# Optimization experiments

Measured on AMD Instinct MI355X. Metric: run time of the kernel, lower is better.

## Reference

```python
import jax, jax.numpy as jnp
import numpy as np

DIM = 192
HEADS = 6
G = 16          # window size (ds_flag=0 dense attention)
B = 1
H_SZ = 256
W_SZ = 256
POS_DIM = 12    # (dim//4)//4
HIDDEN = 768    # 4*dim


def _ln(x, g, b, eps=1e-5):
    m = jnp.mean(x, -1, keepdims=True)
    v = jnp.var(x, -1, keepdims=True)
    return (x - m) / jnp.sqrt(v + eps) * g + b


def setup_inputs() -> dict:
    key = jax.random.key(0)
    ks = jax.random.split(key, 8)
    s = 0.05
    return {
        "x": jax.random.normal(ks[0], (B, H_SZ * W_SZ, DIM), jnp.float32),
        "gamma1": jnp.ones((DIM,), jnp.float32),
        "beta1": jnp.zeros((DIM,), jnp.float32),
        "qkv_w": jax.random.normal(ks[1], (DIM, 3 * DIM), jnp.float32) * s,
        "qkv_b": jnp.zeros((3 * DIM,), jnp.float32),
        "proj_w": jax.random.normal(ks[2], (DIM, DIM), jnp.float32) * s,
        "proj_b": jnp.zeros((DIM,), jnp.float32),
        "pos_proj_w": jax.random.normal(ks[3], (2, POS_DIM), jnp.float32) * s,
        "pos_proj_b": jnp.zeros((POS_DIM,), jnp.float32),
        "ln1_g": jnp.ones((POS_DIM,), jnp.float32),
        "ln1_b": jnp.zeros((POS_DIM,), jnp.float32),
        "pos1_w": jax.random.normal(ks[4], (POS_DIM, POS_DIM), jnp.float32) * s,
        "pos1_b": jnp.zeros((POS_DIM,), jnp.float32),
        "ln2_g": jnp.ones((POS_DIM,), jnp.float32),
        "ln2_b": jnp.zeros((POS_DIM,), jnp.float32),
        "pos2_w": jax.random.normal(ks[5], (POS_DIM, POS_DIM), jnp.float32) * s,
        "pos2_b": jnp.zeros((POS_DIM,), jnp.float32),
        "ln3_g": jnp.ones((POS_DIM,), jnp.float32),
        "ln3_b": jnp.zeros((POS_DIM,), jnp.float32),
        "pos3_w": jax.random.normal(ks[6], (POS_DIM, HEADS), jnp.float32) * s,
        "pos3_b": jnp.zeros((HEADS,), jnp.float32),
        "gamma2": jnp.ones((DIM,), jnp.float32),
        "beta2": jnp.zeros((DIM,), jnp.float32),
        "fc1_w": jax.random.normal(ks[7], (DIM, HIDDEN), jnp.float32) * s,
        "fc1_b": jnp.zeros((HIDDEN,), jnp.float32),
        "fc2_w": jax.random.normal(jax.random.fold_in(key, 9), (HIDDEN, DIM), jnp.float32) * s,
        "fc2_b": jnp.zeros((DIM,), jnp.float32),
        "H": H_SZ,
        "W": W_SZ,
    }


def reference(x, gamma1, beta1, qkv_w, qkv_b, proj_w, proj_b,
              pos_proj_w, pos_proj_b, ln1_g, ln1_b, pos1_w, pos1_b,
              ln2_g, ln2_b, pos2_w, pos2_b, ln3_g, ln3_b, pos3_w, pos3_b,
              gamma2, beta2, fc1_w, fc1_b, fc2_w, fc2_b, H, W):
    Bx, L, C = x.shape
    h = HEADS
    d = C // h
    N = G * G
    shortcut = x
    xn = _ln(x, gamma1, beta1)
    # window partition (H, W divisible by G -> no padding, attn_mask=None)
    xw = xn.reshape(Bx, H // G, G, W // G, G, C).transpose(0, 1, 3, 2, 4, 5)
    xw = xw.reshape(-1, N, C)                       # [B_, N, C]
    B_ = xw.shape[0]
    qkv = (xw @ qkv_w + qkv_b).reshape(B_, N, 3, h, d)
    q = qkv[:, :, 0].transpose(0, 2, 1, 3) * (d ** -0.5)   # [B_, h, N, d]
    k = qkv[:, :, 1].transpose(0, 2, 1, 3)
    v = qkv[:, :, 2].transpose(0, 2, 1, 3)
    attn = jnp.einsum('bhnd,bhmd->bhnm', q, k)      # [B_, h, N, N]
    # dynamic relative position bias (DynamicPosBias MLP + gather)
    r = jnp.arange(1 - G, G)
    biases = jnp.stack(jnp.meshgrid(r, r, indexing='ij')).reshape(2, -1).T.astype(x.dtype)  # [(2G-1)^2, 2]
    p = biases @ pos_proj_w + pos_proj_b
    p = jax.nn.relu(_ln(p, ln1_g, ln1_b)) @ pos1_w + pos1_b
    p = jax.nn.relu(_ln(p, ln2_g, ln2_b)) @ pos2_w + pos2_b
    p = jax.nn.relu(_ln(p, ln3_g, ln3_b)) @ pos3_w + pos3_b  # [(2G-1)^2, heads]
    c = jnp.stack(jnp.meshgrid(jnp.arange(G), jnp.arange(G), indexing='ij')).reshape(2, -1)
    rel = c[:, :, None] - c[:, None, :]             # [2, N, N]
    idx = (rel[0] + G - 1) * (2 * G - 1) + (rel[1] + G - 1)  # [N, N]
    attn = attn + p[idx].transpose(2, 0, 1)[None]   # add [1, h, N, N] bias
    attn = jax.nn.softmax(attn, axis=-1)
    out = jnp.einsum('bhnm,bhmd->bhnd', attn, v).transpose(0, 2, 1, 3).reshape(B_, N, C)
    out = out @ proj_w + proj_b
    # window reverse
    out = out.reshape(Bx, H // G, W // G, G, G, C).transpose(0, 1, 3, 2, 4, 5).reshape(Bx, L, C)
    x = shortcut + out
    y = _ln(x, gamma2, beta2)
    y = jax.nn.gelu(y @ fc1_w + fc1_b, approximate=False) @ fc2_w + fc2_b
    return x + y
```

## Files before the change

### kernel.cpp

```cpp
#include <hip/hip_runtime.h>
#include <hip/hip_bf16.h>

#define DIM 192
#define HEADS 6
#define QKV_N 576
#define HIDDEN 768
#define M_ROWS 65536

typedef unsigned short ushortT;
typedef __attribute__((ext_vector_type(8))) short short8v;
typedef __attribute__((ext_vector_type(4))) float f32x4;
typedef __attribute__((ext_vector_type(4))) unsigned int u32x4;

#define QSCALE_L2E 0.2550348649f
#define LOG2E 1.4426950408889634f

__device__ __forceinline__ float bf2f(ushortT u) {
    union { unsigned int i; float f; } c; c.i = ((unsigned int)u) << 16; return c.f;
}
__device__ __forceinline__ ushortT f2bf(float f) {
    union { float f; unsigned int i; } c; c.f = f;
    unsigned int i = c.i;
    return (ushortT)((i + 0x7fffu + ((i >> 16) & 1u)) >> 16);
}

#define GLOBAL_LOAD_LDS16(gp, lp) \
    __builtin_amdgcn_global_load_lds((const __attribute__((address_space(1))) void*)(gp), \
                                     (__attribute__((address_space(3))) void*)(lp), 16, 0, 0)

__device__ __forceinline__ void ln_relu_mm12(const float* in, const float* g, const float* b,
                                             const float* w, const float* bb, float* out, int nout) {
    float m = 0.f;
#pragma unroll
    for (int j = 0; j < 12; ++j) m += in[j];
    m *= (1.0f / 12.0f);
    float v = 0.f;
#pragma unroll
    for (int j = 0; j < 12; ++j) { float d = in[j] - m; v += d * d; }
    v *= (1.0f / 12.0f);
    float r = rsqrtf(v + 1e-5f);
    float t[12];
#pragma unroll
    for (int j = 0; j < 12; ++j) t[j] = fmaxf((in[j] - m) * r * g[j] + b[j], 0.0f);
    for (int j2 = 0; j2 < nout; ++j2) {
        float s = bb[j2];
#pragma unroll
        for (int j = 0; j < 12; ++j) s = fmaf(t[j], w[j * nout + j2], s);
        out[j2] = s;
    }
}

__global__ __launch_bounds__(256) void prep_kernel(
        const float* __restrict__ qkv_w, const float* __restrict__ proj_w,
        const float* __restrict__ fc1_w, const float* __restrict__ fc2_w,
        ushortT* __restrict__ qkv_wt, ushortT* __restrict__ proj_wt,
        ushortT* __restrict__ fc1_wt, ushortT* __restrict__ fc2_wt,
        const float* __restrict__ pw, const float* __restrict__ pb,
        const float* __restrict__ g1, const float* __restrict__ b1,
        const float* __restrict__ w1, const float* __restrict__ bb1,
        const float* __restrict__ g2, const float* __restrict__ b2,
        const float* __restrict__ w2, const float* __restrict__ bb2,
        const float* __restrict__ g3, const float* __restrict__ b3,
        const float* __restrict__ w3, const float* __restrict__ bb3,
        float* __restrict__ BTf) {
    __shared__ float tile[32][33];
    int blk = blockIdx.x;
    int t = threadIdx.x;
    if (blk < 432) {
        const float* W; ushortT* Wt; int K, N, bx, by;
        if (blk < 108)      { W = qkv_w;  Wt = qkv_wt;  K = 192; N = 576; bx = blk % 18;        by = blk / 18; }
        else if (blk < 144) { int r = blk - 108; W = proj_w; Wt = proj_wt; K = 192; N = 192; bx = r % 6;  by = r / 6; }
        else if (blk < 288) { int r = blk - 144; W = fc1_w;  Wt = fc1_wt;  K = 192; N = 768; bx = r % 24; by = r / 24; }
        else                { int r = blk - 288; W = fc2_w;  Wt = fc2_wt;  K = 768; N = 192; bx = r % 6;  by = r / 6; }
        int tx = t & 31, ty = t >> 5;
        int bX = bx * 32, bY = by * 32;
#pragma unroll
        for (int i = 0; i < 32; i += 8)
            tile[ty + i][tx] = W[(size_t)(bY + ty + i) * N + bX + tx];
        __syncthreads();
#pragma unroll
        for (int i = 0; i < 32; i += 8)
            Wt[(size_t)(bX + ty + i) * K + bY + tx] = f2bf(tile[tx][ty + i]);
    } else {
        int blk2 = blk - 432;
        int h = blk2 >> 8, q = blk2 & 255, kv = t;
        float di = (float)((q >> 4) - (kv >> 4));
        float dj = (float)((q & 15) - (kv & 15));
        float a[12], hh[12];
#pragma unroll
        for (int j = 0; j < 12; ++j) a[j] = di * pw[j] + dj * pw[12 + j] + pb[j];
        ln_relu_mm12(a, g1, b1, w1, bb1, hh, 12);
        ln_relu_mm12(hh, g2, b2, w2, bb2, a, 12);
        float m = 0.f;
#pragma unroll
        for (int j = 0; j < 12; ++j) m += a[j];
        m *= (1.0f / 12.0f);
        float v = 0.f;
#pragma unroll
        for (int j = 0; j < 12; ++j) { float d = a[j] - m; v += d * d; }
        v *= (1.0f / 12.0f);
        float r = rsqrtf(v + 1e-5f);
        float s = bb3[h];
#pragma unroll
        for (int j = 0; j < 12; ++j)
            s = fmaf(fmaxf((a[j] - m) * r * g3[j] + b3[j], 0.0f), w3[j * 6 + h], s);
        int wid = q >> 6, mf = (q >> 4) & 3, l4 = (q >> 2) & 3, rr = q & 3;
        int kc = kv >> 5, cc = kv & 31;
        int cf = (cc >> 4) & 1, l15 = cc & 15;
        int lane = l4 * 16 + l15;
        size_t off = ((size_t)((h * 8 + kc) * 32 + wid * 8 + mf * 2 + cf)) * 256 + lane * 4 + rr;
        BTf[off] = s * LOG2E;
    }
}

__global__ __launch_bounds__(256) void ln_kernel(const float* __restrict__ x,
                                                 const float* __restrict__ g,
                                                 const float* __restrict__ b,
                                                 ushortT* __restrict__ out) {
    int lane = threadIdx.x & 63;
    size_t row = (size_t)blockIdx.x * 4 + (threadIdx.x >> 6);
    const float* xr = x + row * DIM;
    float v0 = xr[lane], v1 = xr[lane + 64], v2 = xr[lane + 128];
    float s = v0 + v1 + v2;
    float ss = v0 * v0 + v1 * v1 + v2 * v2;
#pragma unroll
    for (int off = 32; off > 0; off >>= 1) {
        s += __shfl_xor(s, off);
        ss += __shfl_xor(ss, off);
    }
    float mean = s * (1.0f / DIM);
    float rstd = rsqrtf(ss * (1.0f / DIM) - mean * mean + 1e-5f);
    ushortT* o = out + row * DIM;
    o[lane]       = f2bf((v0 - mean) * rstd * g[lane]       + b[lane]);
    o[lane + 64]  = f2bf((v1 - mean) * rstd * g[lane + 64]  + b[lane + 64]);
    o[lane + 128] = f2bf((v2 - mean) * rstd * g[lane + 128] + b[lane + 128]);
}

template <int MODE, int NY>
__global__ __launch_bounds__(256) void mfma_gemm(const ushortT* __restrict__ A,
                                                 const ushortT* __restrict__ Wt,
                                                 const float* __restrict__ bias,
                                                 const float* __restrict__ resid,
                                                 void* __restrict__ outp,
                                                 int N, int K) {
    __shared__ ushortT As[128 * 64];
    __shared__ ushortT Bs[64 * 64];
    int tid = threadIdx.x;
    int lane = tid & 63, wid = tid >> 6;
    int l15 = lane & 15, l4 = lane >> 4;
    int wr = wid >> 1, wc = wid & 1;
    int p = blockIdx.x;
    int cpx = gridDim.x >> 3;
    int logical = (p & 7) * cpx + (p >> 3);
    int bx = logical / NY;
    int by = logical - bx * NY;
    int bm = bx * 128, bn = by * 64;

    f32x4 acc[4][2];
#pragma unroll
    for (int mf = 0; mf < 4; ++mf)
#pragma unroll
        for (int nf = 0; nf < 2; ++nf)
#pragma unroll
            for (int r = 0; r < 4; ++r) acc[mf][nf][r] = 0.f;

    int srow = tid >> 3;
    int schunk = (tid & 7) ^ (srow & 7);
    const ushortT* agp = A + (size_t)(bm + srow) * K + schunk * 8;
    const ushortT* bgp = Wt + (size_t)(bn + srow) * K + schunk * 8;

    for (int k0 = 0; k0 < K; k0 += 64) {
#pragma unroll
        for (int i = 0; i < 4; ++i)
            GLOBAL_LOAD_LDS16(agp + (size_t)i * 32 * K + k0, As + i * 2048 + wid * 512);
#pragma unroll
        for (int i = 0; i < 2; ++i)
            GLOBAL_LOAD_LDS16(bgp + (size_t)i * 32 * K + k0, Bs + i * 2048 + wid * 512);
        __syncthreads();
#pragma unroll
        for (int ks = 0; ks < 2; ++ks) {
            short8v af[4], bf[2];
#pragma unroll
            for (int mf = 0; mf < 4; ++mf) {
                int row = wr * 64 + mf * 16 + l15;
                af[mf] = *(const short8v*)&As[row * 64 + (((ks * 4 + l4) ^ (l15 & 7)) << 3)];
            }
#pragma unroll
            for (int nf = 0; nf < 2; ++nf) {
                int row = wc * 32 + nf * 16 + l15;
                bf[nf] = *(const short8v*)&Bs[row * 64 + (((ks * 4 + l4) ^ (l15 & 7)) << 3)];
            }
#pragma unroll
            for (int mf = 0; mf < 4; ++mf)
#pragma unroll
                for (int nf = 0; nf < 2; ++nf)
                    acc[mf][nf] = __builtin_amdgcn_mfma_f32_16x16x32_bf16(af[mf], bf[nf], acc[mf][nf], 0, 0, 0);
        }
        __syncthreads();
    }
#pragma unroll
    for (int mf = 0; mf < 4; ++mf) {
        size_t row = (size_t)bm + wr * 64 + mf * 16 + l4 * 4;
#pragma unroll
        for (int nf = 0; nf < 2; ++nf) {
            int col = bn + wc * 32 + nf * 16 + l15;
            float bv = bias[col];
#pragma unroll
            for (int r = 0; r < 4; ++r) {
                size_t off = (row + r) * (size_t)N + col;
                float v = acc[mf][nf][r] + bv;
                if (MODE == 0) {
                    if (col < 192) v *= QSCALE_L2E;
                    ((ushortT*)outp)[off] = f2bf(v);
                } else if (MODE == 1) {
                    float x3 = v * v * v;
                    float z = fmaf(x3, -0.1029537917f, v * -2.302205077f);
                    float e = exp2f(z);
                    v = v * __builtin_amdgcn_rcpf(1.0f + e);
                    ((ushortT*)outp)[off] = f2bf(v);
                } else if (MODE == 2) {
                    ((float*)outp)[off] = resid[off] + v;
                } else {
                    ((float*)outp)[off] += v;
                }
            }
        }
    }
}

__global__ __launch_bounds__(256) void attn_mfma_kernel(const ushortT* __restrict__ qkv,
                                                        const float* __restrict__ BTf,
                                                        ushortT* __restrict__ O) {
    __shared__ ushortT Vt[32][264];
    __shared__ unsigned int Ps[4][64][20];
    int wh = blockIdx.x;
    int w = wh / 6, h = wh - w * 6;
    int wi = w >> 4, wj = w & 15;
    int tid = threadIdx.x, lane = tid & 63, wid = tid >> 6;
    int l15 = lane & 15, l4 = lane >> 4;

    {
        int t = tid;
        int pcol = (t & ~31) | (((t & 15) << 1) | ((t >> 4) & 1));
        size_t gr = (size_t)((wi * 16 + (t >> 4)) * 256 + wj * 16 + (t & 15));
        const ushortT* vp = qkv + gr * 576 + 384 + h * 32;
#pragma unroll
        for (int d0 = 0; d0 < 32; d0 += 8) {
            short8v u = *(const short8v*)(vp + d0);
#pragma unroll
            for (int j = 0; j < 8; ++j) Vt[d0 + j][pcol] = (ushortT)u[j];
        }
    }
    short8v qf[4];
    int qbase = wid * 64;
#pragma unroll
    for (int mf = 0; mf < 4; ++mf) {
        int q = qbase + mf * 16 + l15;
        size_t gr = (size_t)((wi * 16 + (q >> 4)) * 256 + wj * 16 + (q & 15));
        qf[mf] = *(const short8v*)(qkv + gr * 576 + h * 32 + l4 * 8);
    }
    __syncthreads();

    float l_run[4][4];
    f32x4 accO[4][2];
#pragma unroll
    for (int mf = 0; mf < 4; ++mf)
#pragma unroll
        for (int r = 0; r < 4; ++r) {
            l_run[mf][r] = 0.f;
            accO[mf][0][r] = 0.f;
            accO[mf][1][r] = 0.f;
        }
    const float* btb = BTf + ((size_t)(h * 8) * 32 + wid * 8) * 256 + lane * 4;

    auto load_kf = [&](int kc, short8v* kf) {
#pragma unroll
        for (int cf = 0; cf < 2; ++cf) {
            int kv = kc * 32 + cf * 16 + l15;
            size_t gr = (size_t)((wi * 16 + (kv >> 4)) * 256 + wj * 16 + (kv & 15));
            kf[cf] = *(const short8v*)(qkv + gr * 576 + 192 + h * 32 + l4 * 8);
        }
    };

    short8v kfA[2], kfB[2];
    load_kf(0, kfA);

    for (int kc = 0; kc < 8; ++kc) {
        if (kc < 7) load_kf(kc + 1, kfB);
        f32x4 s[4][2];
#pragma unroll
        for (int mf = 0; mf < 4; ++mf)
#pragma unroll
            for (int cf = 0; cf < 2; ++cf)
                s[mf][cf] = *(const f32x4*)(btb + (size_t)(kc * 32 + mf * 2 + cf) * 256);
        __builtin_amdgcn_s_setprio(1);
#pragma unroll
        for (int mf = 0; mf < 4; ++mf)
#pragma unroll
            for (int cf = 0; cf < 2; ++cf)
                s[mf][cf] = __builtin_amdgcn_mfma_f32_16x16x32_bf16(qf[mf], kfA[cf], s[mf][cf], 0, 0, 0);
        __builtin_amdgcn_s_setprio(0);
#pragma unroll
        for (int mf = 0; mf < 4; ++mf) {
#pragma unroll
            for (int r = 0; r < 4; ++r) {
                float p0 = exp2f(s[mf][0][r]);
                float p1 = exp2f(s[mf][1][r]);
                l_run[mf][r] += p0 + p1;
                unsigned int pk;
                asm("v_cvt_pk_bf16_f32 %0, %1, %2" : "=v"(pk) : "v"(p0), "v"(p1));
                Ps[wid][mf * 16 + 4 * l4 + r][l15] = pk;
            }
        }
        short8v vb[2];
#pragma unroll
        for (int nf = 0; nf < 2; ++nf)
            vb[nf] = *(const short8v*)&Vt[nf * 16 + l15][kc * 32 + l4 * 8];
        __builtin_amdgcn_s_setprio(1);
#pragma unroll
        for (int mf = 0; mf < 4; ++mf) {
            u32x4 pr = *(const u32x4*)&Ps[wid][mf * 16 + l15][l4 * 4];
            short8v pa = __builtin_bit_cast(short8v, pr);
#pragma unroll
            for (int nf = 0; nf < 2; ++nf)
                accO[mf][nf] = __builtin_amdgcn_mfma_f32_16x16x32_bf16(pa, vb[nf], accO[mf][nf], 0, 0, 0);
        }
        __builtin_amdgcn_s_setprio(0);
        kfA[0] = kfB[0]; kfA[1] = kfB[1];
    }
#pragma unroll
    for (int mf = 0; mf < 4; ++mf)
#pragma unroll
        for (int r = 0; r < 4; ++r) {
            float l = l_run[mf][r];
            l += __shfl_xor(l, 1);
            l += __shfl_xor(l, 2);
            l += __shfl_xor(l, 4);
            l += __shfl_xor(l, 8);
            l_run[mf][r] = 1.0f / l;
        }
#pragma unroll
    for (int mf = 0; mf < 4; ++mf) {
        int q0 = qbase + mf * 16 + 4 * l4;
#pragma unroll
        for (int r = 0; r < 4; ++r) {
            int q = q0 + r;
            size_t gr = (size_t)((wi * 16 + (q >> 4)) * 256 + wj * 16 + (q & 15));
            ushortT* op = O + gr * 192 + h * 32 + l15;
            float inv = l_run[mf][r];
            op[0]  = f2bf(accO[mf][0][r] * inv);
            op[16] = f2bf(accO[mf][1][r] * inv);
        }
    }
}

extern "C" void kernel_launch(void* const* d_in, const int* in_sizes, int n_in,
                              void* d_out, int out_size, void* d_ws, size_t ws_size,
                              hipStream_t stream) {
    const float* x        = (const float*)d_in[0];
    const float* gamma1   = (const float*)d_in[1];
    const float* beta1    = (const float*)d_in[2];
    const float* qkv_w    = (const float*)d_in[3];
    const float* qkv_b    = (const float*)d_in[4];
    const float* proj_w   = (const float*)d_in[5];
    const float* proj_b   = (const float*)d_in[6];
    const float* pos_proj_w = (const float*)d_in[7];
    const float* pos_proj_b = (const float*)d_in[8];
    const float* ln1_g    = (const float*)d_in[9];
    const float* ln1_b    = (const float*)d_in[10];
    const float* pos1_w   = (const float*)d_in[11];
    const float* pos1_b   = (const float*)d_in[12];
    const float* ln2_g    = (const float*)d_in[13];
    const float* ln2_b    = (const float*)d_in[14];
    const float* pos2_w   = (const float*)d_in[15];
    const float* pos2_b   = (const float*)d_in[16];
    const float* ln3_g    = (const float*)d_in[17];
    const float* ln3_b    = (const float*)d_in[18];
    const float* pos3_w   = (const float*)d_in[19];
    const float* pos3_b   = (const float*)d_in[20];
    const float* gamma2   = (const float*)d_in[21];
    const float* beta2    = (const float*)d_in[22];
    const float* fc1_w    = (const float*)d_in[23];
    const float* fc1_b    = (const float*)d_in[24];
    const float* fc2_w    = (const float*)d_in[25];
    const float* fc2_b    = (const float*)d_in[26];
    float* out = (float*)d_out;

    char* ws = (char*)d_ws;
    ushortT* qkv = (ushortT*)(ws + 0);
    ushortT* y1  = (ushortT*)(ws + 0);
    ushortT* xn   = (ushortT*)(ws + 100663296);
    ushortT* Obuf = xn;
    ushortT* xn2  = xn;
    ushortT* qkv_wt  = (ushortT*)(ws + 125829120);
    ushortT* proj_wt = (ushortT*)(ws + 126050304);
    ushortT* fc1_wt  = (ushortT*)(ws + 126124032);
    ushortT* fc2_wt  = (ushortT*)(ws + 126418944);
    float*   BTf     = (float*)(ws + 126713856);

    prep_kernel<<<1968, 256, 0, stream>>>(
        qkv_w, proj_w, fc1_w, fc2_w, qkv_wt, proj_wt, fc1_wt, fc2_wt,
        pos_proj_w, pos_proj_b, ln1_g, ln1_b, pos1_w, pos1_b,
        ln2_g, ln2_b, pos2_w, pos2_b, ln3_g, ln3_b, pos3_w, pos3_b, BTf);
    ln_kernel<<<M_ROWS / 4, 256, 0, stream>>>(x, gamma1, beta1, xn);
    mfma_gemm<0, 9><<<(M_ROWS / 128) * (QKV_N / 64), 256, 0, stream>>>(
        xn, qkv_wt, qkv_b, nullptr, qkv, QKV_N, DIM);
    attn_mfma_kernel<<<1536, 256, 0, stream>>>(qkv, BTf, Obuf);
    mfma_gemm<2, 3><<<(M_ROWS / 128) * (DIM / 64), 256, 0, stream>>>(
        Obuf, proj_wt, proj_b, x, out, DIM, DIM);
    ln_kernel<<<M_ROWS / 4, 256, 0, stream>>>(out, gamma2, beta2, xn2);
    mfma_gemm<1, 12><<<(M_ROWS / 128) * (HIDDEN / 64), 256, 0, stream>>>(
        xn2, fc1_wt, fc1_b, nullptr, y1, HIDDEN, DIM);
    mfma_gemm<3, 3><<<(M_ROWS / 128) * (DIM / 64), 256, 0, stream>>>(
        y1, fc2_wt, fc2_b, nullptr, out, DIM, HIDDEN);
}
```

Baseline: 242.3 us.

## Double-buffer GEMM LDS tiles and prefetch attention bias one chunk ahead

The GEMM kernel now keeps two LDS buffers for A and B and issues the global-to-LDS loads for tile t+1 before computing tile t. Partial vmcnt waits and raw barriers replace the full __syncthreads. K becomes a template parameter so the loop can be unrolled. The attention kernel also loads the relative-position bias for the next key chunk into registers while the current chunk computes. This is meant to hide global load latency, at the cost of twice the GEMM shared memory (possible lower occupancy) and more registers in attention.

After: 232.6 us. -4.0%, faster.

```diff
diff --git a/kernel.cpp b/kernel.cpp
--- a/kernel.cpp
+++ b/kernel.cpp
@@ -136,15 +136,16 @@
     o[lane + 128] = f2bf((v2 - mean) * rstd * g[lane + 128] + b[lane + 128]);
 }
 
-template <int MODE, int NY>
+template <int MODE, int NY, int KK>
 __global__ __launch_bounds__(256) void mfma_gemm(const ushortT* __restrict__ A,
                                                  const ushortT* __restrict__ Wt,
                                                  const float* __restrict__ bias,
                                                  const float* __restrict__ resid,
                                                  void* __restrict__ outp,
-                                                 int N, int K) {
-    __shared__ ushortT As[128 * 64];
-    __shared__ ushortT Bs[64 * 64];
+                                                 int N) {
+    __shared__ ushortT As[2][128 * 64];
+    __shared__ ushortT Bs[2][64 * 64];
+    const int NT = KK / 64;
     int tid = threadIdx.x;
     int lane = tid & 63, wid = tid >> 6;
     int l15 = lane & 15, l4 = lane >> 4;
@@ -166,29 +167,43 @@
 
     int srow = tid >> 3;
     int schunk = (tid & 7) ^ (srow & 7);
-    const ushortT* agp = A + (size_t)(bm + srow) * K + schunk * 8;
-    const ushortT* bgp = Wt + (size_t)(bn + srow) * K + schunk * 8;
-
-    for (int k0 = 0; k0 < K; k0 += 64) {
+    const ushortT* agp = A + (size_t)(bm + srow) * KK + schunk * 8;
+    const ushortT* bgp = Wt + (size_t)(bn + srow) * KK + schunk * 8;
+
+    auto STAGE = [&](int buf, int t) {
+        int k0 = t * 64;
 #pragma unroll
         for (int i = 0; i < 4; ++i)
-            GLOBAL_LOAD_LDS16(agp + (size_t)i * 32 * K + k0, As + i * 2048 + wid * 512);
+            GLOBAL_LOAD_LDS16(agp + (size_t)i * 32 * KK + k0, &As[buf][i * 2048 + wid * 512]);
 #pragma unroll
         for (int i = 0; i < 2; ++i)
-            GLOBAL_LOAD_LDS16(bgp + (size_t)i * 32 * K + k0, Bs + i * 2048 + wid * 512);
-        __syncthreads();
+            GLOBAL_LOAD_LDS16(bgp + (size_t)i * 32 * KK + k0, &Bs[buf][i * 2048 + wid * 512]);
+    };
+
+    STAGE(0, 0);
+    for (int t = 0; t < NT; ++t) {
+        int cur = t & 1;
+        if (t + 1 < NT) {
+            STAGE(cur ^ 1, t + 1);
+            asm volatile("s_waitcnt vmcnt(6)" ::: "memory");
+        } else {
+            asm volatile("s_waitcnt vmcnt(0)" ::: "memory");
+        }
+        __builtin_amdgcn_s_barrier();
+        const ushortT* Asc = As[cur];
+        const ushortT* Bsc = Bs[cur];
 #pragma unroll
         for (int ks = 0; ks < 2; ++ks) {
             short8v af[4], bf[2];
 #pragma unroll
             for (int mf = 0; mf < 4; ++mf) {
                 int row = wr * 64 + mf * 16 + l15;
-                af[mf] = *(const short8v*)&As[row * 64 + (((ks * 4 + l4) ^ (l15 & 7)) << 3)];
+                af[mf] = *(const short8v*)&Asc[row * 64 + (((ks * 4 + l4) ^ (l15 & 7)) << 3)];
             }
 #pragma unroll
             for (int nf = 0; nf < 2; ++nf) {
                 int row = wc * 32 + nf * 16 + l15;
-                bf[nf] = *(const short8v*)&Bs[row * 64 + (((ks * 4 + l4) ^ (l15 & 7)) << 3)];
+                bf[nf] = *(const short8v*)&Bsc[row * 64 + (((ks * 4 + l4) ^ (l15 & 7)) << 3)];
             }
 #pragma unroll
             for (int mf = 0; mf < 4; ++mf)
@@ -196,7 +211,7 @@
                 for (int nf = 0; nf < 2; ++nf)
                     acc[mf][nf] = __builtin_amdgcn_mfma_f32_16x16x32_bf16(af[mf], bf[nf], acc[mf][nf], 0, 0, 0);
         }
-        __syncthreads();
+        __builtin_amdgcn_s_barrier();
     }
 #pragma unroll
     for (int mf = 0; mf < 4; ++mf) {
@@ -282,24 +297,28 @@
         }
     };
 
+    f32x4 bias_buf[8];
+    auto load_bias = [&](int kc) {
+#pragma unroll
+        for (int i = 0; i < 8; ++i)
+            bias_buf[i] = *(const f32x4*)(btb + (size_t)(kc * 32 + i) * 256);
+    };
+
     short8v kfA[2], kfB[2];
     load_kf(0, kfA);
+    load_bias(0);
 
     for (int kc = 0; kc < 8; ++kc) {
         if (kc < 7) load_kf(kc + 1, kfB);
         f32x4 s[4][2];
+        __builtin_amdgcn_s_setprio(1);
 #pragma unroll
         for (int mf = 0; mf < 4; ++mf)
 #pragma unroll
             for (int cf = 0; cf < 2; ++cf)
-                s[mf][cf] = *(const f32x4*)(btb + (size_t)(kc * 32 + mf * 2 + cf) * 256);
-        __builtin_amdgcn_s_setprio(1);
-#pragma unroll
-        for (int mf = 0; mf < 4; ++mf)
-#pragma unroll
-            for (int cf = 0; cf < 2; ++cf)
-                s[mf][cf] = __builtin_amdgcn_mfma_f32_16x16x32_bf16(qf[mf], kfA[cf], s[mf][cf], 0, 0, 0);
+                s[mf][cf] = __builtin_amdgcn_mfma_f32_16x16x32_bf16(qf[mf], kfA[cf], bias_buf[mf * 2 + cf], 0, 0, 0);
         __builtin_amdgcn_s_setprio(0);
+        if (kc < 7) load_bias(kc + 1);
 #pragma unroll
         for (int mf = 0; mf < 4; ++mf) {
 #pragma unroll
@@ -403,14 +422,14 @@
         pos_proj_w, pos_proj_b, ln1_g, ln1_b, pos1_w, pos1_b,
         ln2_g, ln2_b, pos2_w, pos2_b, ln3_g, ln3_b, pos3_w, pos3_b, BTf);
     ln_kernel<<<M_ROWS / 4, 256, 0, stream>>>(x, gamma1, beta1, xn);
-    mfma_gemm<0, 9><<<(M_ROWS / 128) * (QKV_N / 64), 256, 0, stream>>>(
-        xn, qkv_wt, qkv_b, nullptr, qkv, QKV_N, DIM);
+    mfma_gemm<0, 9, 192><<<(M_ROWS / 128) * (QKV_N / 64), 256, 0, stream>>>(
+        xn, qkv_wt, qkv_b, nullptr, qkv, QKV_N);
     attn_mfma_kernel<<<1536, 256, 0, stream>>>(qkv, BTf, Obuf);
-    mfma_gemm<2, 3><<<(M_ROWS / 128) * (DIM / 64), 256, 0, stream>>>(
-        Obuf, proj_wt, proj_b, x, out, DIM, DIM);
+    mfma_gemm<2, 3, 192><<<(M_ROWS / 128) * (DIM / 64), 256, 0, stream>>>(
+        Obuf, proj_wt, proj_b, x, out, DIM);
     ln_kernel<<<M_ROWS / 4, 256, 0, stream>>>(out, gamma2, beta2, xn2);
-    mfma_gemm<1, 12><<<(M_ROWS / 128) * (HIDDEN / 64), 256, 0, stream>>>(
-        xn2, fc1_wt, fc1_b, nullptr, y1, HIDDEN, DIM);
-    mfma_gemm<3, 3><<<(M_ROWS / 128) * (DIM / 64), 256, 0, stream>>>(
-        y1, fc2_wt, fc2_b, nullptr, out, DIM, HIDDEN);
-}
+    mfma_gemm<1, 12, 192><<<(M_ROWS / 128) * (HIDDEN / 64), 256, 0, stream>>>(
+        xn2, fc1_wt, fc1_b, nullptr, y1, HIDDEN);
+    mfma_gemm<3, 3, 768><<<(M_ROWS / 128) * (DIM / 64), 256, 0, stream>>>(
+        y1, fc2_wt, fc2_b, nullptr, out, DIM);
+}
```
